# Optimization experiments

Hardware: AMD Instinct MI355X
Metric: run time of the kernel (lower is better)

The kernel has to match this reference:

```python
import jax, jax.numpy as jnp
import numpy as np

B, N, C, D = 8, 8192, 3, 64
S, K = 2048, 32
EPS = 1e-7       # acos clamp epsilon (matches torch code)
BN_EPS = 1e-5    # torch BatchNorm2d default eps


def _safe_unit(v):
    # v: [..., C]; returns (v/||v|| with 0 where ||v||==0, ||v||).
    # Matches torch's `u[u != u] = 0` NaN fix and has zero grad at v==0.
    sq = jnp.sum(v * v, axis=-1, keepdims=True)
    d = jnp.where(sq > 0, jnp.sqrt(jnp.where(sq > 0, sq, 1.0)), 0.0)
    u = jnp.where(d > 0, v / jnp.where(d > 0, d, 1.0), 0.0)
    return u, d


def _acos_clamped(x):
    return jnp.arccos(jnp.clip(x, -1.0 + EPS, 1.0 - EPS))


def _conv_bn_relu(x, w, b, gamma, beta):
    # x: [B, Cin, K, S]; w: [Cout, Cin] (1x1 Conv2d); BN in training mode (batch stats).
    y = jnp.einsum('oc,bcks->boks', w, x) + b[None, :, None, None]
    mean = jnp.mean(y, axis=(0, 2, 3), keepdims=True)
    var = jnp.mean((y - mean) ** 2, axis=(0, 2, 3), keepdims=True)
    y = (y - mean) / jnp.sqrt(var + BN_EPS)
    y = y * gamma[None, :, None, None] + beta[None, :, None, None]
    return jax.nn.relu(y)


def _forward(contour, LOA, feature_maps,
             fe_w1, fe_b1, fe_g1, fe_be1, fe_w2, fe_b2, fe_g2, fe_be2,
             fl_w1, fl_b1, fl_g1, fl_be1, fl_w2, fl_b2, fl_g2, fl_be2):
    # --- downsampling: uniform linspace indices (torch .long() truncates) ---
    new_index = jnp.linspace(0.0, N - 1, S).astype(jnp.int32)               # [S]
    sampled = contour[:, new_index, :]                                       # [B,S,C]
    new_LOA = LOA[:, new_index, :]                                           # [B,S,C]
    # --- contiguous circular neighborhoods around each sampled index ---
    group_idx = (new_index[:, None] - K // 2 + jnp.arange(K)[None, :]) % N   # [S,K]
    # --- irregular gathers ---
    nb_pts = contour[:, group_idx, :]                                        # [B,S,K,C]
    nb_loa = LOA[:, group_idx, :]                                            # [B,S,K,C]
    local = nb_pts - sampled[:, :, None, :]                                  # [B,S,K,C]
    d1_unit, d1 = _safe_unit(local)
    axis = new_LOA[:, :, None, :]                                            # [B,S,1,C]
    a1 = jnp.sum(d1_unit * axis, axis=-1, keepdims=True)
    a2 = jnp.sum(d1_unit * nb_loa, axis=-1, keepdims=True)
    a3 = _acos_clamped(jnp.sum(nb_loa * axis, axis=-1, keepdims=True))
    # NOTE: torch does `D_0[D_0 == 0] = -1` on a *bool* tensor; bool(-1) is True,
    # so D_0 becomes all-True and D_0.float()*a3 == a3 (sign is always +1).
    inner_vec = local - jnp.roll(local, 1, axis=2)
    inner_unit, _ = _safe_unit(inner_vec)
    a4 = jnp.sum(inner_unit * nb_loa, axis=-1, keepdims=True)
    a5 = jnp.sum(inner_unit * jnp.roll(nb_loa, 1, axis=2), axis=-1, keepdims=True)
    a6 = _acos_clamped(jnp.sum(nb_loa * jnp.roll(nb_loa, 1, axis=2), axis=-1, keepdims=True))
    # same bool-assignment quirk for D_1 -> a6 unchanged
    d2 = _acos_clamped(jnp.sum(d1_unit * jnp.roll(d1_unit, 1, axis=2), axis=-1, keepdims=True))
    rif = jnp.concatenate([d1, d2, a1, a2, a3, a4, a5, a6], axis=-1)         # [B,S,K,8]
    # --- feature enhancement MLP on [B, ch, K, S] layout ---
    x = jnp.transpose(rif, (0, 3, 2, 1))                                     # [B,8,K,S]
    x = _conv_bn_relu(x, fe_w1, fe_b1, fe_g1, fe_be1)                        # [B,32,K,S]
    x = _conv_bn_relu(x, fe_w2, fe_b2, fe_g2, fe_be2)                        # [B,64,K,S]
    # --- gather input feature maps with the same indices, concat channels ---
    fmap = jnp.transpose(feature_maps, (0, 2, 1))                            # [B,N,D]
    grouped = jnp.transpose(fmap[:, group_idx, :], (0, 3, 2, 1))             # [B,D,K,S]
    x = jnp.concatenate([x, grouped], axis=1)                                # [B,128,K,S]
    # --- filter MLP + max over neighborhood ---
    x = _conv_bn_relu(x, fl_w1, fl_b1, fl_g1, fl_be1)                        # [B,128,K,S]
    x = _conv_bn_relu(x, fl_w2, fl_b2, fl_g2, fl_be2)                        # [B,256,K,S]
    out = jnp.max(x, axis=2)                                                 # [B,256,S]
    return sampled, new_LOA, out


def setup_inputs() -> dict:
    key = jax.random.key(0)
    ks = jax.random.split(key, 12)

    def w(k, o, i):
        return jax.random.normal(k, (o, i), jnp.float32) / np.sqrt(i)

    return {
        'contour': jax.random.normal(ks[0], (B, N, C), jnp.float32),
        'LOA': jax.random.normal(ks[1], (B, N, C), jnp.float32),
        'feature_maps': jax.random.normal(ks[2], (B, D, N), jnp.float32),
        'fe_w1': w(ks[3], 32, 8),  'fe_b1': jnp.zeros(32),
        'fe_g1': jnp.ones(32),     'fe_be1': jnp.zeros(32),
        'fe_w2': w(ks[4], 64, 32), 'fe_b2': jnp.zeros(64),
        'fe_g2': jnp.ones(64),     'fe_be2': jnp.zeros(64),
        'fl_w1': w(ks[5], 128, 128), 'fl_b1': jnp.zeros(128),
        'fl_g1': jnp.ones(128),      'fl_be1': jnp.zeros(128),
        'fl_w2': w(ks[6], 256, 128), 'fl_b2': jnp.zeros(256),
        'fl_g2': jnp.ones(256),      'fl_be2': jnp.zeros(256),
    }


def reference(contour, LOA, feature_maps,
              fe_w1, fe_b1, fe_g1, fe_be1, fe_w2, fe_b2, fe_g2, fe_be2,
              fl_w1, fl_b1, fl_g1, fl_be1, fl_w2, fl_b2, fl_g2, fl_be2):
    return _forward(contour, LOA, feature_maps,
                    fe_w1, fe_b1, fe_g1, fe_be1, fe_w2, fe_b2, fe_g2, fe_be2,
                    fl_w1, fl_b1, fl_g1, fl_be1, fl_w2, fl_b2, fl_g2, fl_be2)
```

## Files before the change

### kernel.cpp

```cpp
#include <hip/hip_runtime.h>
#include <stdint.h>

#define NPTS 8192
#define SSZ  2048
#define QTOT (8*2048*32)

#define F_MOM1   4
#define F_MOM2   12
#define F_SC1    972
#define F_SH1    1004
#define F_SC2    1036
#define F_SH2    1100
#define F_SC3    1164
#define F_SH3    1292
#define F_SC4    1420
#define F_SH4    1676
#define F_WF1    1932
#define F_WF2    2188
#define F_G1     53388
#define F_BE1    53420
#define F_G2     53452
#define F_BE2    53516
#define F_G3     53580
#define F_BE3    53708
#define F_G4     53836
#define F_BE4    54092
#define F_M1     57344
#define F_M2     57376
#define F_P      60000
#define F_S3P    77000
#define F_C4P    94000
#define CTR_OFF  524288ull
#define LOA_OFF  1310720ull
#define U3H_OFF  2097152ull
#define U3L_OFF  2129920ull
#define U4H_OFF  2162688ull
#define U4L_OFF  2228224ull
#define U2H_OFF  2293760ull
#define U2L_OFF  2297856ull
#define H2H_OFF  2301952ull
#define H2L_OFF  (2301952ull + 67108864ull)
#define WS_H2    (2301952ull + 2ull*67108864ull)

typedef __attribute__((ext_vector_type(8))) short s8v;
typedef __attribute__((ext_vector_type(4))) short s4v;
typedef __attribute__((ext_vector_type(4))) float f4v;
typedef __attribute__((ext_vector_type(4))) float fl4;
#define MFMA(a,b,c) __builtin_amdgcn_mfma_f32_16x16x32_bf16(a,b,c,0,0,0)

__device__ inline float bf2f(unsigned short u){ return __uint_as_float(((uint32_t)u)<<16); }
__device__ inline unsigned short f2bf(float f){
    uint32_t x=__float_as_uint(f);
    return (unsigned short)((x + 0x7fffu + ((x>>16)&1u))>>16);
}
__device__ inline float clipf(float x){
    const float LO=(float)(-1.0+1e-7), HI=(float)(1.0-1e-7);
    return fminf(fmaxf(x,LO),HI);
}
__device__ inline float wredsum(float v){
#pragma unroll
    for(int m=1;m<64;m<<=1) v+=__shfl_xor(v,m,64);
    return v;
}
__device__ inline float ldin(const void* p,size_t i,int md){
    return md ? ((const float*)p)[i] : bf2f(((const unsigned short*)p)[i]);
}
__device__ inline int sidx(int s){ return (s*8191)/2047; }

__global__ void k_detect(const void* contour,int* flag){
    __shared__ int he;
    if(threadIdx.x==0) he=0;
    __syncthreads();
    const unsigned short* u=(const unsigned short*)contour;
    int h=0;
    for(int i=threadIdx.x;i<4096;i+=256){
        unsigned short lo=u[2*i];
        if(((lo>>7)&0xFF)>=0x86) h++;
    }
    atomicAdd(&he,h);
    __syncthreads();
    if(threadIdx.x==0) *flag = (he>400) ? 1 : 0;
}

__global__ __launch_bounds__(256) void k_convert(
    const void* ctr,const void* loa,
    const void* w1,const void* w2,const void* w3,const void* w4,
    const void* g1,const void* be1,const void* g2,const void* be2,
    const void* g3,const void* be3,const void* g4,const void* be4,
    float* F, float* ctrf, float* loaf,
    unsigned short* u2h, unsigned short* u2l,
    unsigned short* u3h, unsigned short* u3l,
    unsigned short* u4h, unsigned short* u4l,
    float* out)
{
    int md=((const int*)F)[0];
    int i = blockIdx.x*256+threadIdx.x;
    ctrf[i]=ldin(ctr,i,md);
    loaf[i]=ldin(loa,i,md);
    if(i<16384){
        int b=i>>11, s=i&2047;
        int idx=sidx(s);
        size_t cb=((size_t)b*NPTS+idx)*3;
        size_t ob=(size_t)i*3;
        out[ob]        =ldin(ctr,cb  ,md);
        out[ob+1]      =ldin(ctr,cb+1,md);
        out[ob+2]      =ldin(ctr,cb+2,md);
        out[49152+ob]  =ldin(loa,cb  ,md);
        out[49152+ob+1]=ldin(loa,cb+1,md);
        out[49152+ob+2]=ldin(loa,cb+2,md);
    }
    if(i<256)  F[F_WF1+i]=ldin(w1,i,md);
    if(i<2048) F[F_WF2+i]=ldin(w2,i,md);
    if(i<2048){
        int j=i&7, lane=(i>>3)&63, mt=i>>9;
        int m=lane&15, kk=((lane>>4)<<3)|j;
        float w=ldin(w2,(size_t)(mt*16+m)*32 + kk, md);
        unsigned short hi=f2bf(w);
        u2h[i]=hi; u2l[i]=f2bf(w-bf2f(hi));
    }
    if(i<16384){
        int j=i&7, lane=(i>>3)&63, kt=(i>>9)&3, mt=i>>11;
        int m=lane&15, kk=((lane>>4)<<3)|j;
        float w=ldin(w3,(size_t)(mt*16+m)*128 + kt*32+kk, md);
        unsigned short hi=f2bf(w);
        u3h[i]=hi; u3l[i]=f2bf(w-bf2f(hi));
    }
    if(i<32768){
        int j=i&7, lane=(i>>3)&63, kt=(i>>9)&3, mt=i>>11;
        int m=lane&15, kk=((lane>>4)<<3)|j;
        float w=ldin(w4,(size_t)(mt*16+m)*128 + kt*32+kk, md);
        unsigned short hi=f2bf(w);
        u4h[i]=hi; u4l[i]=f2bf(w-bf2f(hi));
    }
    if(i<968)   F[4+i]=0.f;
    if(i<16896) F[F_P+i]=0.f;
    if(i<16384) F[F_S3P+i]=0.f;
    if(i<32768) F[F_C4P+i]=0.f;
    if(i<32){ F[F_G1+i]=ldin(g1,i,md); F[F_BE1+i]=ldin(be1,i,md); }
    if(i<64){ F[F_G2+i]=ldin(g2,i,md); F[F_BE2+i]=ldin(be2,i,md); }
    if(i<128){ F[F_G3+i]=ldin(g3,i,md); F[F_BE3+i]=ldin(be3,i,md); }
    if(i<256){ F[F_G4+i]=ldin(g4,i,md); F[F_BE4+i]=ldin(be4,i,md); }
}

__device__ inline void rif_compute(const float* __restrict__ ctr,const float* __restrict__ loa,
                                   int b,int s,int k,float r[8])
{
    int idx=sidx(s);
    int gi=(idx-16+k)&(NPTS-1);
    size_t cb=((size_t)b*NPTS+gi)*3;
    float px=ctr[cb],py=ctr[cb+1],pz=ctr[cb+2];
    float lx=loa[cb],ly=loa[cb+1],lz=loa[cb+2];
    float sx=__shfl(px,16,32),sy=__shfl(py,16,32),sz=__shfl(pz,16,32);
    float ax=__shfl(lx,16,32),ay=__shfl(ly,16,32),az=__shfl(lz,16,32);
    float vx=px-sx,vy=py-sy,vz=pz-sz;
    float sq=vx*vx+vy*vy+vz*vz;
    float d1=sq>0.f?sqrtf(sq):0.f;
    float inv=d1>0.f?1.f/d1:0.f;
    float ux=vx*inv,uy=vy*inv,uz=vz*inv;
    float a1=ux*ax+uy*ay+uz*az;
    float a2=ux*lx+uy*ly+uz*lz;
    float a3=acosf(clipf(lx*ax+ly*ay+lz*az));
    int src=(k+31)&31;
    float pvx=__shfl(vx,src,32),pvy=__shfl(vy,src,32),pvz=__shfl(vz,src,32);
    float plx=__shfl(lx,src,32),ply=__shfl(ly,src,32),plz=__shfl(lz,src,32);
    float pux=__shfl(ux,src,32),puy=__shfl(uy,src,32),puz=__shfl(uz,src,32);
    float ivx=vx-pvx,ivy=vy-pvy,ivz=vz-pvz;
    float isq=ivx*ivx+ivy*ivy+ivz*ivz;
    float idn=isq>0.f?1.f/sqrtf(isq):0.f;
    float iux=ivx*idn,iuy=ivy*idn,iuz=ivz*idn;
    float a4=iux*lx+iuy*ly+iuz*lz;
    float a5=iux*plx+iuy*ply+iuz*plz;
    float a6=acosf(clipf(lx*plx+ly*ply+lz*plz));
    float d2=acosf(clipf(ux*pux+uy*puy+uz*puz));
    r[0]=d1;r[1]=d2;r[2]=a1;r[3]=a2;r[4]=a3;r[5]=a4;r[6]=a5;r[7]=a6;
}

__global__ __launch_bounds__(256) void k_features(
    const float* __restrict__ ctrf,const float* __restrict__ loaf,
    float* __restrict__ mom1,float* __restrict__ mom2)
{
    __shared__ float sm1[8],sm2[64];
    int t=threadIdx.x;
    if(t<8)sm1[t]=0.f;
    if(t<64)sm2[t]=0.f;
    __syncthreads();
    int lane=t&63,k=t&31;
    int q=blockIdx.x*256+t;
    int pos=q>>5,b=pos>>11,s=pos&2047;
    float r[8];
    rif_compute(ctrf,loaf,b,s,k,r);
#pragma unroll
    for(int i=0;i<8;i++){ float sv=wredsum(r[i]); if(lane==0)atomicAdd(&sm1[i],sv); }
#pragma unroll
    for(int i=0;i<8;i++)
#pragma unroll
        for(int j=i;j<8;j++){ float sv=wredsum(r[i]*r[j]); if(lane==0)atomicAdd(&sm2[i*8+j],sv); }
    __syncthreads();
    if(t<8)atomicAdd(&mom1[t],sm1[t]);
    if(t<64)atomicAdd(&mom2[t],sm2[t]);
}

__global__ void k_bn1(float* F){
    int o=threadIdx.x;
    if(o>=32)return;
    const float invP=1.0f/(float)QTOT;
    float m[8],w[8];
#pragma unroll
    for(int c=0;c<8;c++){ m[c]=F[F_MOM1+c]*invP; w[c]=F[F_WF1+o*8+c]; }
    float Ey=0.f;
#pragma unroll
    for(int c=0;c<8;c++) Ey+=w[c]*m[c];
    float Eyy=0.f;
#pragma unroll
    for(int i=0;i<8;i++)
#pragma unroll
        for(int j=0;j<8;j++){
            int a=i<j?i:j,bb=i<j?j:i;
            Eyy+=w[i]*w[j]*F[F_MOM2+a*8+bb]*invP;
        }
    float var=fmaxf(Eyy-Ey*Ey,0.f);
    float sc=F[F_G1+o]/sqrtf(var+1e-5f);
    F[F_SC1+o]=sc;
    F[F_SH1+o]=F[F_BE1+o]-Ey*sc;
}

#define S2T 264
__global__ __launch_bounds__(256) void k_stats2m(
    const float* __restrict__ ctrf,const float* __restrict__ loaf,
    const float* __restrict__ F,float* __restrict__ P)
{
    __shared__ unsigned short TH[32*S2T];
    __shared__ unsigned short TL[32*S2T];
    int t=threadIdx.x, wv=t>>6, lane=t&63;
    int quad=lane>>4, col=lane&15;
    int mi=wv>>1, ni=wv&1;
    float acc8[8];
#pragma unroll
    for(int k=0;k<8;k++) acc8[k]=0.f;
    f4v Z; Z[0]=0.f;Z[1]=0.f;Z[2]=0.f;Z[3]=0.f;
    f4v C0=Z, C1=Z;
    const float* wf1=F+F_WF1;
    const float* sc1=F+F_SC1; const float* sh1=F+F_SH1;
    for(int tt=0;tt<2;++tt){
        int tile=blockIdx.x*2+tt;
        int pos=tile*8 + wv*2 + (lane>>5);
        int b=pos>>11, s=pos&2047;
        float r[8]; rif_compute(ctrf,loaf,b,s,lane&31,r);
        int mypos=wv*64+lane;
#pragma unroll
        for(int c=0;c<32;c++){
            const float* w=wf1+c*8;
            float y=w[0]*r[0]+w[1]*r[1]+w[2]*r[2]+w[3]*r[3]
                   +w[4]*r[4]+w[5]*r[5]+w[6]*r[6]+w[7]*r[7];
            float h=fmaxf(y*sc1[c]+sh1[c],0.f);
            unsigned short hi=f2bf(h);
            TH[c*S2T+mypos]=hi;
            TL[c*S2T+mypos]=f2bf(h-bf2f(hi));
        }
        __syncthreads();
#pragma unroll
        for(int kt=0;kt<8;kt++){
            s8v AH=*(const s8v*)(TH+(mi*16+col)*S2T + kt*32 + quad*8);
            s8v AL=*(const s8v*)(TL+(mi*16+col)*S2T + kt*32 + quad*8);
            s8v BH=*(const s8v*)(TH+(ni*16+col)*S2T + kt*32 + quad*8);
            s8v BL=*(const s8v*)(TL+(ni*16+col)*S2T + kt*32 + quad*8);
            if(kt&1){
                C1=MFMA(AH,BH,C1); C1=MFMA(AH,BL,C1); C1=MFMA(AL,BH,C1);
            }else{
                C0=MFMA(AH,BH,C0); C0=MFMA(AH,BL,C0); C0=MFMA(AL,BH,C0);
            }
        }
#pragma unroll
        for(int k=0;k<8;k++){
            int c=wv*8+k;
            const unsigned short* ph=TH+c*S2T+lane*4;
            const unsigned short* pl=TL+c*S2T+lane*4;
            acc8[k]+=bf2f(ph[0])+bf2f(ph[1])+bf2f(ph[2])+bf2f(ph[3])
                    +bf2f(pl[0])+bf2f(pl[1])+bf2f(pl[2])+bf2f(pl[3]);
        }
        __syncthreads();
    }
    float* Ps=P+(size_t)(blockIdx.x&15)*1056;
#pragma unroll
    for(int rg=0;rg<4;rg++){
        float v=C0[rg]+C1[rg];
        atomicAdd(&Ps[32+(mi*16+quad*4+rg)*32 + ni*16+col], v);
    }
#pragma unroll
    for(int k=0;k<8;k++){
        float sv=wredsum(acc8[k]);
        if(lane==0) atomicAdd(&Ps[wv*8+k],sv);
    }
}

__global__ void k_red(float* F){
    int t=threadIdx.x;
    for(int e=t;e<1056;e+=256){
        float s=0.f;
#pragma unroll
        for(int k=0;k<16;k++) s+=F[F_P+k*1056+e];
        if(e<32) F[F_M1+e]=s; else F[F_M2+e-32]=s;
    }
    __syncthreads();
    int o=t;
    if(o<64){
        const float invP=1.0f/(float)QTOT;
        const float* w=F+F_WF2+o*32;
        const float* M2=F+F_M2;
        float Ey=0.f;
#pragma unroll
        for(int c=0;c<32;c++) Ey+=w[c]*F[F_M1+c];
        Ey*=invP;
        float Eyy=0.f;
        for(int c1=0;c1<32;c1++){
            float acc=0.f;
#pragma unroll
            for(int c2=0;c2<32;c2++) acc+=w[c2]*M2[c1*32+c2];
            Eyy+=w[c1]*acc;
        }
        Eyy*=invP;
        float var=fmaxf(Eyy-Ey*Ey,0.f);
        float s=F[F_G2+o]/sqrtf(var+1e-5f);
        F[F_SC2+o]=s;
        F[F_SH2+o]=F[F_BE2+o]-Ey*s;
    }
}

__global__ void k_bnd3(float* F){
    int o=threadIdx.x;
    if(o>=128)return;
    float sum=0.f,ssq=0.f;
    for(int s=0;s<64;s++){
        sum+=F[F_S3P+s*256+o];
        ssq+=F[F_S3P+s*256+128+o];
    }
    const float invP=1.0f/(float)QTOT;
    float mean=sum*invP;
    float var=fmaxf(ssq*invP-mean*mean,0.f);
    float sc=F[F_G3+o]/sqrtf(var+1e-5f);
    F[F_SC3+o]=sc;
    F[F_SH3+o]=F[F_BE3+o]-mean*sc;
}

__global__ void k_bnd4(float* F){
    int o=threadIdx.x;
    if(o>=256)return;
    float sum=0.f,ssq=0.f;
    for(int s=0;s<64;s++){
        sum+=F[F_C4P+s*512+o];
        ssq+=F[F_C4P+s*512+256+o];
    }
    const float invP=1.0f/(float)QTOT;
    float mean=sum*invP;
    float var=fmaxf(ssq*invP-mean*mean,0.f);
    float sc=F[F_G4+o]/sqrtf(var+1e-5f);
    F[F_SC4+o]=sc;
    F[F_SH4+o]=F[F_BE4+o]-mean*sc;
}

#define XST 136

__device__ inline void build_x2_8(
    const float* __restrict__ ctrf,const float* __restrict__ loaf,
    const void* __restrict__ fm,const float* __restrict__ F,
    const unsigned short* __restrict__ u2h,const unsigned short* __restrict__ u2l,
    int md,int b,int s0,int wv,int lane,
    unsigned short* XH,unsigned short* XL)
{
    int quad=lane>>4, col=lane&15;
    if(wv<4){
        float r8[8]; rif_compute(ctrf,loaf,b,s0+(lane>>5),lane&31,r8);
        const float* wf1=F+F_WF1;
        const float* sc1=F+F_SC1; const float* sh1=F+F_SH1;
        s8v vh,vl;
#pragma unroll
        for(int j=0;j<8;j++){
            int o=8*wv+j;
            const float* w=wf1+o*8;
            float y=w[0]*r8[0]+w[1]*r8[1]+w[2]*r8[2]+w[3]*r8[3]
                   +w[4]*r8[4]+w[5]*r8[5]+w[6]*r8[6]+w[7]*r8[7];
            float h=fmaxf(y*sc1[o]+sh1[o],0.f);
            unsigned short hi=f2bf(h);
            vh[j]=(short)hi;
            vl[j]=(short)f2bf(h-bf2f(hi));
        }
        *(s8v*)(XH + lane*XST + 8*wv)=vh;
        *(s8v*)(XL + lane*XST + 8*wv)=vl;
    }else{
        int dbase=16*(wv-4);
        int s=s0+(lane>>5), k=lane&31;
        int gi=(sidx(s)-16+k)&(NPTS-1);
        size_t fb=(size_t)b*64*NPTS+gi;
        for(int g=0;g<2;g++){
            s8v vh,vl;
#pragma unroll
            for(int j=0;j<8;j++){
                int d=dbase+g*8+j;
                float v = md ? ((const float*)fm)[fb+(size_t)d*NPTS]
                             : bf2f(((const unsigned short*)fm)[fb+(size_t)d*NPTS]);
                unsigned short hi=f2bf(v);
                vh[j]=(short)hi;
                vl[j]=(short)f2bf(v-bf2f(hi));
            }
            *(s8v*)(XH + lane*XST + 64 + dbase + g*8)=vh;
            *(s8v*)(XL + lane*XST + 64 + dbase + g*8)=vl;
        }
    }
    __syncthreads();
    int cg=wv>>1, nb=(wv&1)*2;
    s8v AH=*(const s8v*)(u2h+(cg*64+lane)*8);
    s8v AL=*(const s8v*)(u2l+(cg*64+lane)*8);
    s8v BH0=*(const s8v*)(XH+((nb  )*16+col)*XST+quad*8);
    s8v BL0=*(const s8v*)(XL+((nb  )*16+col)*XST+quad*8);
    s8v BH1=*(const s8v*)(XH+((nb+1)*16+col)*XST+quad*8);
    s8v BL1=*(const s8v*)(XL+((nb+1)*16+col)*XST+quad*8);
    f4v Z; Z[0]=0.f;Z[1]=0.f;Z[2]=0.f;Z[3]=0.f;
    f4v c0=MFMA(AH,BH0,Z), c1=MFMA(AH,BH1,Z);
    c0=MFMA(AH,BL0,c0); c1=MFMA(AH,BL1,c1);
    c0=MFMA(AL,BH0,c0); c1=MFMA(AL,BH1,c1);
    __syncthreads();
    const float* sc2=F+F_SC2; const float* sh2=F+F_SH2;
    int chb=cg*16+quad*4;
    float g0=sc2[chb],g1=sc2[chb+1],g2=sc2[chb+2],g3=sc2[chb+3];
    float b0=sh2[chb],b1=sh2[chb+1],b2=sh2[chb+2],b3=sh2[chb+3];
#pragma unroll
    for(int i=0;i<2;i++){
        f4v c = i? c1 : c0;
        int p=(nb+i)*16+col;
        float v0=fmaxf(c[0]*g0+b0,0.f);
        float v1=fmaxf(c[1]*g1+b1,0.f);
        float v2=fmaxf(c[2]*g2+b2,0.f);
        float v3=fmaxf(c[3]*g3+b3,0.f);
        unsigned short h0=f2bf(v0),h1=f2bf(v1),h2=f2bf(v2),h3=f2bf(v3);
        s4v vh,vl;
        vh[0]=(short)h0; vh[1]=(short)h1; vh[2]=(short)h2; vh[3]=(short)h3;
        vl[0]=(short)f2bf(v0-bf2f(h0)); vl[1]=(short)f2bf(v1-bf2f(h1));
        vl[2]=(short)f2bf(v2-bf2f(h2)); vl[3]=(short)f2bf(v3-bf2f(h3));
        *(s4v*)(XH + p*XST + chb)=vh;
        *(s4v*)(XL + p*XST + chb)=vl;
    }
}

#define G1_STEP8(UH,UL) \
    for(int kt=0;kt<4;kt++){ \
        s8v BH[4],BL[4]; \
        for(int nt=0;nt<4;nt++){ \
            int boff=(nt*16+col)*XST + kt*32 + quad*8; \
            BH[nt]=*(const s8v*)(XH+boff); \
            BL[nt]=*(const s8v*)(XL+boff); \
        } \
        { \
            s8v AH=*(const s8v*)(UH+((wv*4+kt)*64+lane)*8); \
            s8v AL=*(const s8v*)(UL+((wv*4+kt)*64+lane)*8); \
            for(int nt=0;nt<4;nt++) C[nt]=MFMA(AH,BH[nt],C[nt]); \
            for(int nt=0;nt<4;nt++) C[nt]=MFMA(AH,BL[nt],C[nt]); \
            for(int nt=0;nt<4;nt++) C[nt]=MFMA(AL,BH[nt],C[nt]); \
        } \
    }

#define G2_STEP8(UH,UL) \
    for(int kt=0;kt<4;kt++){ \
        s8v BH[4],BL[4]; \
        for(int nt=0;nt<4;nt++){ \
            int boff=(nt*16+col)*XST + kt*32 + quad*8; \
            BH[nt]=*(const s8v*)(XH+boff); \
            BL[nt]=*(const s8v*)(XL+boff); \
        } \
        for(int mi=0;mi<2;mi++){ \
            int mt=2*wv+mi; \
            s8v AH=*(const s8v*)(UH+((mt*4+kt)*64+lane)*8); \
            s8v AL=*(const s8v*)(UL+((mt*4+kt)*64+lane)*8); \
            for(int nt=0;nt<4;nt++) C2[mi][nt]=MFMA(AH,BH[nt],C2[mi][nt]); \
            for(int nt=0;nt<4;nt++) C2[mi][nt]=MFMA(AH,BL[nt],C2[mi][nt]); \
            for(int nt=0;nt<4;nt++) C2[mi][nt]=MFMA(AL,BH[nt],C2[mi][nt]); \
        } \
    }

__global__ __launch_bounds__(512) void k_stats3(
    const float* __restrict__ ctrf,const float* __restrict__ loaf,
    const void* __restrict__ fm,float* __restrict__ F,
    const unsigned short* __restrict__ u2h,const unsigned short* __restrict__ u2l,
    const unsigned short* __restrict__ u3h,const unsigned short* __restrict__ u3l,
    unsigned short* __restrict__ h2h,unsigned short* __restrict__ h2l)
{
    __shared__ unsigned short XH[64*XST];
    __shared__ unsigned short XL[64*XST];
    __shared__ float as_[128],qs_[128];
    int t=threadIdx.x, wv=t>>6, lane=t&63;
    if(t<128){as_[t]=0.f;qs_[t]=0.f;}
    int md=((const int*)F)[0];
    int pos0=blockIdx.x*2, b=pos0>>11, s0=pos0&2047;
    build_x2_8(ctrf,loaf,fm,F,u2h,u2l,md,b,s0,wv,lane,XH,XL);
    __syncthreads();
    int quad=lane>>4, col=lane&15;
    f4v Z; Z[0]=0.f;Z[1]=0.f;Z[2]=0.f;Z[3]=0.f;
    f4v C[4];
#pragma unroll
    for(int nt=0;nt<4;nt++) C[nt]=Z;
#pragma unroll
    G1_STEP8(u3h,u3l)
    if(h2h){
        int pos=t>>3, off=((t&7)^(pos&7))*8;
        size_t go=(size_t)blockIdx.x*4096 + (size_t)pos*64 + off;
        *(s8v*)(h2h+go)=*(const s8v*)(XH+pos*XST+off);
        *(s8v*)(h2l+go)=*(const s8v*)(XL+pos*XST+off);
    }
#pragma unroll
    for(int rg=0;rg<4;rg++){
        float sm=0.f,sq=0.f;
#pragma unroll
        for(int nt=0;nt<4;nt++){ float v=C[nt][rg]; sm+=v; sq+=v*v; }
        sm+=__shfl_xor(sm,1); sq+=__shfl_xor(sq,1);
        sm+=__shfl_xor(sm,2); sq+=__shfl_xor(sq,2);
        sm+=__shfl_xor(sm,4); sq+=__shfl_xor(sq,4);
        sm+=__shfl_xor(sm,8); sq+=__shfl_xor(sq,8);
        if(col==0){
            int ch=wv*16+quad*4+rg;
            atomicAdd(&as_[ch],sm); atomicAdd(&qs_[ch],sq);
        }
    }
    __syncthreads();
    float* Ps=F+F_S3P+(size_t)(blockIdx.x&63)*256;
    if(t<128){atomicAdd(&Ps[t],as_[t]);atomicAdd(&Ps[128+t],qs_[t]);}
}

__global__ __launch_bounds__(512) void k_conv4h(
    const void* __restrict__ fm,float* __restrict__ F,
    const unsigned short* __restrict__ u3h,const unsigned short* __restrict__ u3l,
    const unsigned short* __restrict__ u4h,const unsigned short* __restrict__ u4l,
    const unsigned short* __restrict__ h2h,const unsigned short* __restrict__ h2l,
    float* __restrict__ maxb)
{
    __shared__ unsigned short XH[64*XST];
    __shared__ unsigned short XL[64*XST];
    __shared__ float as_[256],qs_[256];
    int t=threadIdx.x, wv=t>>6, lane=t&63;
    if(t<256){as_[t]=0.f; qs_[t]=0.f;}
    int md=((const int*)F)[0];
    int pos0=blockIdx.x*2, b=pos0>>11, s0=pos0&2047;
    {
        int pos=t>>3, off=((t&7)^(pos&7))*8;
        size_t go=(size_t)blockIdx.x*4096 + (size_t)pos*64 + off;
        *(s8v*)(XH+pos*XST+off)=*(const s8v*)(h2h+go);
        *(s8v*)(XL+pos*XST+off)=*(const s8v*)(h2l+go);
    }
    {
        int dbase=8*wv;
        int s=s0+(lane>>5), k=lane&31;
        int gi=(sidx(s)-16+k)&(NPTS-1);
        size_t fb=(size_t)b*64*NPTS+gi;
        s8v vh,vl;
#pragma unroll
        for(int j=0;j<8;j++){
            int d=dbase+j;
            float v = md ? ((const float*)fm)[fb+(size_t)d*NPTS]
                         : bf2f(((const unsigned short*)fm)[fb+(size_t)d*NPTS]);
            unsigned short hi=f2bf(v);
            vh[j]=(short)hi;
            vl[j]=(short)f2bf(v-bf2f(hi));
        }
        *(s8v*)(XH + lane*XST + 64 + dbase)=vh;
        *(s8v*)(XL + lane*XST + 64 + dbase)=vl;
    }
    __syncthreads();
    int quad=lane>>4, col=lane&15;
    f4v Z; Z[0]=0.f;Z[1]=0.f;Z[2]=0.f;Z[3]=0.f;
    f4v C[4];
#pragma unroll
    for(int nt=0;nt<4;nt++) C[nt]=Z;
#pragma unroll
    G1_STEP8(u3h,u3l)
    __syncthreads();
    const float* sc3=F+F_SC3; const float* sh3=F+F_SH3;
    {
        int chb=wv*16+quad*4;
#pragma unroll
        for(int nt=0;nt<4;nt++){
            int p=nt*16+col;
            s4v vh,vl;
#pragma unroll
            for(int rg=0;rg<4;rg++){
                float v=C[nt][rg];
                v=fmaxf(v*sc3[chb+rg]+sh3[chb+rg],0.f);
                unsigned short hi=f2bf(v);
                vh[rg]=(short)hi;
                vl[rg]=(short)f2bf(v-bf2f(hi));
            }
            *(s4v*)(XH + p*XST + chb)=vh;
            *(s4v*)(XL + p*XST + chb)=vl;
        }
    }
    __syncthreads();
    f4v C2[2][4];
#pragma unroll
    for(int mi=0;mi<2;mi++)
#pragma unroll
        for(int nt=0;nt<4;nt++) C2[mi][nt]=Z;
#pragma unroll
    G2_STEP8(u4h,u4l)
#pragma unroll
    for(int mi=0;mi<2;mi++){
        int mt=2*wv+mi;
#pragma unroll
        for(int rg=0;rg<4;rg++){
            float sm=0.f,sq=0.f,mx0=-3.4e38f,mx1=-3.4e38f;
#pragma unroll
            for(int nt=0;nt<4;nt++){
                float v=C2[mi][nt][rg];
                sm+=v; sq+=v*v;
                if(nt<2) mx0=fmaxf(mx0,v); else mx1=fmaxf(mx1,v);
            }
            sm+=__shfl_xor(sm,1); sq+=__shfl_xor(sq,1);
            sm+=__shfl_xor(sm,2); sq+=__shfl_xor(sq,2);
            sm+=__shfl_xor(sm,4); sq+=__shfl_xor(sq,4);
            sm+=__shfl_xor(sm,8); sq+=__shfl_xor(sq,8);
            mx0=fmaxf(mx0,__shfl_xor(mx0,1)); mx1=fmaxf(mx1,__shfl_xor(mx1,1));
            mx0=fmaxf(mx0,__shfl_xor(mx0,2)); mx1=fmaxf(mx1,__shfl_xor(mx1,2));
            mx0=fmaxf(mx0,__shfl_xor(mx0,4)); mx1=fmaxf(mx1,__shfl_xor(mx1,4));
            mx0=fmaxf(mx0,__shfl_xor(mx0,8)); mx1=fmaxf(mx1,__shfl_xor(mx1,8));
            if(col==0){
                int ch=mt*16+quad*4+rg;
                atomicAdd(&as_[ch],sm); atomicAdd(&qs_[ch],sq);
                size_t ob=((size_t)b*256+ch)*SSZ + s0;
                maxb[ob]=mx0; maxb[ob+1]=mx1;
            }
        }
    }
    __syncthreads();
    float* Ps=F+F_C4P+(size_t)(blockIdx.x&63)*512;
    if(t<256){atomicAdd(&Ps[t],as_[t]);atomicAdd(&Ps[256+t],qs_[t]);}
}

__global__ __launch_bounds__(512) void k_conv4(
    const float* __restrict__ ctrf,const float* __restrict__ loaf,
    const void* __restrict__ fm,float* __restrict__ F,
    const unsigned short* __restrict__ u2h,const unsigned short* __restrict__ u2l,
    const unsigned short* __restrict__ u3h,const unsigned short* __restrict__ u3l,
    const unsigned short* __restrict__ u4h,const unsigned short* __restrict__ u4l,
    float* __restrict__ maxb)
{
    __shared__ unsigned short XH[64*XST];
    __shared__ unsigned short XL[64*XST];
    __shared__ float as_[256],qs_[256];
    int t=threadIdx.x, wv=t>>6, lane=t&63;
    if(t<256){as_[t]=0.f; qs_[t]=0.f;}
    int md=((const int*)F)[0];
    int pos0=blockIdx.x*2, b=pos0>>11, s0=pos0&2047;
    build_x2_8(ctrf,loaf,fm,F,u2h,u2l,md,b,s0,wv,lane,XH,XL);
    __syncthreads();
    int quad=lane>>4, col=lane&15;
    f4v Z; Z[0]=0.f;Z[1]=0.f;Z[2]=0.f;Z[3]=0.f;
    f4v C[4];
#pragma unroll
    for(int nt=0;nt<4;nt++) C[nt]=Z;
#pragma unroll
    G1_STEP8(u3h,u3l)
    __syncthreads();
    const float* sc3=F+F_SC3; const float* sh3=F+F_SH3;
    {
        int chb=wv*16+quad*4;
#pragma unroll
        for(int nt=0;nt<4;nt++){
            int p=nt*16+col;
            s4v vh,vl;
#pragma unroll
            for(int rg=0;rg<4;rg++){
                float v=C[nt][rg];
                v=fmaxf(v*sc3[chb+rg]+sh3[chb+rg],0.f);
                unsigned short hi=f2bf(v);
                vh[rg]=(short)hi;
                vl[rg]=(short)f2bf(v-bf2f(hi));
            }
            *(s4v*)(XH + p*XST + chb)=vh;
            *(s4v*)(XL + p*XST + chb)=vl;
        }
    }
    __syncthreads();
    f4v C2[2][4];
#pragma unroll
    for(int mi=0;mi<2;mi++)
#pragma unroll
        for(int nt=0;nt<4;nt++) C2[mi][nt]=Z;
#pragma unroll
    G2_STEP8(u4h,u4l)
#pragma unroll
    for(int mi=0;mi<2;mi++){
        int mt=2*wv+mi;
#pragma unroll
        for(int rg=0;rg<4;rg++){
            float sm=0.f,sq=0.f,mx0=-3.4e38f,mx1=-3.4e38f;
#pragma unroll
            for(int nt=0;nt<4;nt++){
                float v=C2[mi][nt][rg];
                sm+=v; sq+=v*v;
                if(nt<2) mx0=fmaxf(mx0,v); else mx1=fmaxf(mx1,v);
            }
            sm+=__shfl_xor(sm,1); sq+=__shfl_xor(sq,1);
            sm+=__shfl_xor(sm,2); sq+=__shfl_xor(sq,2);
            sm+=__shfl_xor(sm,4); sq+=__shfl_xor(sq,4);
            sm+=__shfl_xor(sm,8); sq+=__shfl_xor(sq,8);
            mx0=fmaxf(mx0,__shfl_xor(mx0,1)); mx1=fmaxf(mx1,__shfl_xor(mx1,1));
            mx0=fmaxf(mx0,__shfl_xor(mx0,2)); mx1=fmaxf(mx1,__shfl_xor(mx1,2));
            mx0=fmaxf(mx0,__shfl_xor(mx0,4)); mx1=fmaxf(mx1,__shfl_xor(mx1,4));
            mx0=fmaxf(mx0,__shfl_xor(mx0,8)); mx1=fmaxf(mx1,__shfl_xor(mx1,8));
            if(col==0){
                int ch=mt*16+quad*4+rg;
                atomicAdd(&as_[ch],sm); atomicAdd(&qs_[ch],sq);
                size_t ob=((size_t)b*256+ch)*SSZ + s0;
                maxb[ob]=mx0; maxb[ob+1]=mx1;
            }
        }
    }
    __syncthreads();
    float* Ps=F+F_C4P+(size_t)(blockIdx.x&63)*512;
    if(t<256){atomicAdd(&Ps[t],as_[t]);atomicAdd(&Ps[256+t],qs_[t]);}
}

__global__ __launch_bounds__(256) void k_apply(
    const float* __restrict__ F,float* __restrict__ out)
{
    int e4=blockIdx.x*256+threadIdx.x;
    int j=(e4>>9)&255;
    float sc=F[F_SC4+j],sh=F[F_SH4+j];
    fl4* p=(fl4*)(out+98304)+e4;
    fl4 v=*p;
    v[0]=fmaxf(v[0]*sc+sh,0.f);
    v[1]=fmaxf(v[1]*sc+sh,0.f);
    v[2]=fmaxf(v[2]*sc+sh,0.f);
    v[3]=fmaxf(v[3]*sc+sh,0.f);
    *p=v;
}

extern "C" void kernel_launch(void* const* d_in, const int* in_sizes, int n_in,
                              void* d_out, int out_size, void* d_ws, size_t ws_size,
                              hipStream_t stream)
{
    const void* contour=d_in[0];
    const void* loa    =d_in[1];
    const void* fm     =d_in[2];
    const void* w1 =d_in[3];  const void* g1 =d_in[5];  const void* be1=d_in[6];
    const void* w2 =d_in[7];  const void* g2 =d_in[9];  const void* be2=d_in[10];
    const void* w3 =d_in[11]; const void* g3 =d_in[13]; const void* be3=d_in[14];
    const void* w4 =d_in[15]; const void* g4 =d_in[17]; const void* be4=d_in[18];
    float* out=(float*)d_out;

    float* F=(float*)d_ws;
    char* base=(char*)d_ws;
    float* ctrf=(float*)(base+CTR_OFF);
    float* loaf=(float*)(base+LOA_OFF);
    unsigned short* u3h=(unsigned short*)(base+U3H_OFF);
    unsigned short* u3l=(unsigned short*)(base+U3L_OFF);
    unsigned short* u4h=(unsigned short*)(base+U4H_OFF);
    unsigned short* u4l=(unsigned short*)(base+U4L_OFF);
    unsigned short* u2h=(unsigned short*)(base+U2H_OFF);
    unsigned short* u2l=(unsigned short*)(base+U2L_OFF);
    int tier = (ws_size >= WS_H2) ? 1 : 0;
    unsigned short* h2h = tier==1 ? (unsigned short*)(base+H2H_OFF) : (unsigned short*)0;
    unsigned short* h2l = tier==1 ? (unsigned short*)(base+H2L_OFF) : (unsigned short*)0;
    float* maxb=out+98304;

    k_detect<<<1,256,0,stream>>>(contour,(int*)d_ws);
    k_convert<<<768,256,0,stream>>>(contour,loa,w1,w2,w3,w4,g1,be1,g2,be2,g3,be3,g4,be4,
                                    F,ctrf,loaf,u2h,u2l,u3h,u3l,u4h,u4l,out);
    k_features<<<2048,256,0,stream>>>(ctrf,loaf,F+F_MOM1,F+F_MOM2);
    k_bn1<<<1,32,0,stream>>>(F);
    k_stats2m<<<1024,256,0,stream>>>(ctrf,loaf,F,F+F_P);
    k_red<<<1,256,0,stream>>>(F);
    k_stats3<<<8192,512,0,stream>>>(ctrf,loaf,fm,F,u2h,u2l,u3h,u3l,h2h,h2l);
    k_bnd3<<<1,128,0,stream>>>(F);
    if(tier==1){
        k_conv4h<<<8192,512,0,stream>>>(fm,F,u3h,u3l,u4h,u4l,h2h,h2l,maxb);
    }else{
        k_conv4<<<8192,512,0,stream>>>(ctrf,loaf,fm,F,u2h,u2l,u3h,u3l,u4h,u4l,maxb);
    }
    k_bnd4<<<1,256,0,stream>>>(F);
    k_apply<<<4096,256,0,stream>>>(F,out);
}
```

Measured before the change: 635.8 us.

## Cache layer-3 conv outputs in bf16 instead of recomputing from cached inputs

The stats kernel now stores the pre-BN layer-3 conv outputs (128 channels per position) as single bf16 values in workspace. The final conv kernel reads these directly, applies BN and ReLU, and skips reloading the feature maps and redoing the layer-3 GEMM. This removes a full GEMM pass plus the irregular feature-map gathers. The cost is that the intermediate is stored at bf16 precision rather than the previous hi/lo split, so accuracy may drop.

```diff
diff --git a/kernel.cpp b/kernel.cpp
--- a/kernel.cpp
+++ b/kernel.cpp
@@ -38,9 +38,8 @@
 #define U4L_OFF  2228224ull
 #define U2H_OFF  2293760ull
 #define U2L_OFF  2297856ull
-#define H2H_OFF  2301952ull
-#define H2L_OFF  (2301952ull + 67108864ull)
-#define WS_H2    (2301952ull + 2ull*67108864ull)
+#define Y3_OFF   2301952ull
+#define WS_T1    (2301952ull + 134217728ull)
 
 typedef __attribute__((ext_vector_type(8))) short s8v;
 typedef __attribute__((ext_vector_type(4))) short s4v;
@@ -481,7 +480,7 @@
     const void* __restrict__ fm,float* __restrict__ F,
     const unsigned short* __restrict__ u2h,const unsigned short* __restrict__ u2l,
     const unsigned short* __restrict__ u3h,const unsigned short* __restrict__ u3l,
-    unsigned short* __restrict__ h2h,unsigned short* __restrict__ h2l)
+    unsigned short* __restrict__ y3)
 {
     __shared__ unsigned short XH[64*XST];
     __shared__ unsigned short XL[64*XST];
@@ -499,11 +498,14 @@
     for(int nt=0;nt<4;nt++) C[nt]=Z;
 #pragma unroll
     G1_STEP8(u3h,u3l)
-    if(h2h){
-        int pos=t>>3, off=((t&7)^(pos&7))*8;
-        size_t go=(size_t)blockIdx.x*4096 + (size_t)pos*64 + off;
-        *(s8v*)(h2h+go)=*(const s8v*)(XH+pos*XST+off);
-        *(s8v*)(h2l+go)=*(const s8v*)(XL+pos*XST+off);
+    if(y3){
+#pragma unroll
+        for(int nt=0;nt<4;nt++){
+            s4v v4;
+#pragma unroll
+            for(int rg=0;rg<4;rg++) v4[rg]=(short)f2bf(C[nt][rg]);
+            *(s4v*)(y3 + (size_t)blockIdx.x*8192 + (size_t)(wv*4+nt)*256 + lane*4) = v4;
+        }
     }
 #pragma unroll
     for(int rg=0;rg<4;rg++){
@@ -524,11 +526,10 @@
     if(t<128){atomicAdd(&Ps[t],as_[t]);atomicAdd(&Ps[128+t],qs_[t]);}
 }
 
-__global__ __launch_bounds__(512) void k_conv4h(
-    const void* __restrict__ fm,float* __restrict__ F,
-    const unsigned short* __restrict__ u3h,const unsigned short* __restrict__ u3l,
+__global__ __launch_bounds__(512) void k_conv4y(
+    float* __restrict__ F,
     const unsigned short* __restrict__ u4h,const unsigned short* __restrict__ u4l,
-    const unsigned short* __restrict__ h2h,const unsigned short* __restrict__ h2l,
+    const unsigned short* __restrict__ y3,
     float* __restrict__ maxb)
 {
     __shared__ unsigned short XH[64*XST];
@@ -536,61 +537,30 @@
     __shared__ float as_[256],qs_[256];
     int t=threadIdx.x, wv=t>>6, lane=t&63;
     if(t<256){as_[t]=0.f; qs_[t]=0.f;}
-    int md=((const int*)F)[0];
+    int quad=lane>>4, col=lane&15;
     int pos0=blockIdx.x*2, b=pos0>>11, s0=pos0&2047;
-    {
-        int pos=t>>3, off=((t&7)^(pos&7))*8;
-        size_t go=(size_t)blockIdx.x*4096 + (size_t)pos*64 + off;
-        *(s8v*)(XH+pos*XST+off)=*(const s8v*)(h2h+go);
-        *(s8v*)(XL+pos*XST+off)=*(const s8v*)(h2l+go);
-    }
-    {
-        int dbase=8*wv;
-        int s=s0+(lane>>5), k=lane&31;
-        int gi=(sidx(s)-16+k)&(NPTS-1);
-        size_t fb=(size_t)b*64*NPTS+gi;
-        s8v vh,vl;
-#pragma unroll
-        for(int j=0;j<8;j++){
-            int d=dbase+j;
-            float v = md ? ((const float*)fm)[fb+(size_t)d*NPTS]
-                         : bf2f(((const unsigned short*)fm)[fb+(size_t)d*NPTS]);
-            unsigned short hi=f2bf(v);
-            vh[j]=(short)hi;
-            vl[j]=(short)f2bf(v-bf2f(hi));
-        }
-        *(s8v*)(XH + lane*XST + 64 + dbase)=vh;
-        *(s8v*)(XL + lane*XST + 64 + dbase)=vl;
-    }
-    __syncthreads();
-    int quad=lane>>4, col=lane&15;
-    f4v Z; Z[0]=0.f;Z[1]=0.f;Z[2]=0.f;Z[3]=0.f;
-    f4v C[4];
-#pragma unroll
-    for(int nt=0;nt<4;nt++) C[nt]=Z;
-#pragma unroll
-    G1_STEP8(u3h,u3l)
-    __syncthreads();
     const float* sc3=F+F_SC3; const float* sh3=F+F_SH3;
     {
         int chb=wv*16+quad*4;
 #pragma unroll
         for(int nt=0;nt<4;nt++){
-            int p=nt*16+col;
+            s4v v4=*(const s4v*)(y3 + (size_t)blockIdx.x*8192 + (size_t)(wv*4+nt)*256 + lane*4);
             s4v vh,vl;
 #pragma unroll
             for(int rg=0;rg<4;rg++){
-                float v=C[nt][rg];
+                float v=bf2f((unsigned short)v4[rg]);
                 v=fmaxf(v*sc3[chb+rg]+sh3[chb+rg],0.f);
                 unsigned short hi=f2bf(v);
                 vh[rg]=(short)hi;
                 vl[rg]=(short)f2bf(v-bf2f(hi));
             }
+            int p=nt*16+col;
             *(s4v*)(XH + p*XST + chb)=vh;
             *(s4v*)(XL + p*XST + chb)=vl;
         }
     }
     __syncthreads();
+    f4v Z; Z[0]=0.f;Z[1]=0.f;Z[2]=0.f;Z[3]=0.f;
     f4v C2[2][4];
 #pragma unroll
     for(int mi=0;mi<2;mi++)
@@ -754,9 +724,8 @@
     unsigned short* u4l=(unsigned short*)(base+U4L_OFF);
     unsigned short* u2h=(unsigned short*)(base+U2H_OFF);
     unsigned short* u2l=(unsigned short*)(base+U2L_OFF);
-    int tier = (ws_size >= WS_H2) ? 1 : 0;
-    unsigned short* h2h = tier==1 ? (unsigned short*)(base+H2H_OFF) : (unsigned short*)0;
-    unsigned short* h2l = tier==1 ? (unsigned short*)(base+H2L_OFF) : (unsigned short*)0;
+    int tier = (ws_size >= WS_T1) ? 1 : 0;
+    unsigned short* y3 = tier==1 ? (unsigned short*)(base+Y3_OFF) : (unsigned short*)0;
     float* maxb=out+98304;
 
     k_detect<<<1,256,0,stream>>>(contour,(int*)d_ws);
@@ -766,10 +735,10 @@
     k_bn1<<<1,32,0,stream>>>(F);
     k_stats2m<<<1024,256,0,stream>>>(ctrf,loaf,F,F+F_P);
     k_red<<<1,256,0,stream>>>(F);
-    k_stats3<<<8192,512,0,stream>>>(ctrf,loaf,fm,F,u2h,u2l,u3h,u3l,h2h,h2l);
+    k_stats3<<<8192,512,0,stream>>>(ctrf,loaf,fm,F,u2h,u2l,u3h,u3l,y3);
     k_bnd3<<<1,128,0,stream>>>(F);
     if(tier==1){
-        k_conv4h<<<8192,512,0,stream>>>(fm,F,u3h,u3l,u4h,u4l,h2h,h2l,maxb);
+        k_conv4y<<<8192,512,0,stream>>>(F,u4h,u4l,y3,maxb);
     }else{
         k_conv4<<<8192,512,0,stream>>>(ctrf,loaf,fm,F,u2h,u2l,u3h,u3l,u4h,u4l,maxb);
     }
```

Result: faster. 591.5 us (-7.0%).
